# Kernel optimization log

Measured on AMD Instinct MI355X. Metric: run time of the kernel, lower is better.

## Reference

```python
import jax, jax.numpy as jnp
import numpy as np

NEG_SLOPE = 0.2  # PyG GATConv default LeakyReLU slope


def gat_layer(x, src, dst, W, a_src, a_dst, bias, heads, out_dim, concat, n_nodes):
    # x: [N, F_in]; W: [F_in, heads*out_dim]
    h = (x @ W).reshape(n_nodes, heads, out_dim)          # [N, H, C]
    alpha_src = jnp.sum(h * a_src, axis=-1)               # [N, H]
    alpha_dst = jnp.sum(h * a_dst, axis=-1)               # [N, H]
    e = jax.nn.leaky_relu(alpha_src[src] + alpha_dst[dst], NEG_SLOPE)  # [E, H]
    # softmax over edges grouped by destination node (self-loops guarantee nonempty segments)
    m = jax.ops.segment_max(e, dst, num_segments=n_nodes)  # [N, H]
    w = jnp.exp(e - m[dst])
    s = jax.ops.segment_sum(w, dst, num_segments=n_nodes)  # [N, H]
    alpha = w / s[dst]                                     # [E, H]
    msg = h[src] * alpha[:, :, None]                       # [E, H, C]
    out = jax.ops.segment_sum(msg, dst, num_segments=n_nodes)  # [N, H, C]
    if concat:
        out = out.reshape(n_nodes, heads * out_dim)
    else:
        out = out.mean(axis=1)
    return out + bias


def setup_inputs() -> dict:
    key = jax.random.key(0)
    ks = jax.random.split(key, 12)
    N, E = 50000, 600000
    F_IN, OUT = 256, 64
    H1, C1 = 2, 2 * OUT          # conv1: heads=2, per-head dim 128
    F2 = H1 * C1                 # 256
    x = jax.random.normal(ks[0], (N, F_IN), dtype=jnp.float32)
    edge_index = jax.random.randint(ks[1], (2, E), 0, N, dtype=jnp.int64)
    g1 = 1.0 / np.sqrt(F_IN)
    g2 = 1.0 / np.sqrt(F2)
    return {
        "x": x,
        "edge_index": edge_index,
        "W1": jax.random.normal(ks[2], (F_IN, H1 * C1), dtype=jnp.float32) * g1,
        "a1_src": jax.random.normal(ks[3], (H1, C1), dtype=jnp.float32) * g2,
        "a1_dst": jax.random.normal(ks[4], (H1, C1), dtype=jnp.float32) * g2,
        "b1": jnp.zeros((H1 * C1,), dtype=jnp.float32),
        "W2": jax.random.normal(ks[5], (F2, OUT), dtype=jnp.float32) * g2,
        "a2_src": jax.random.normal(ks[6], (1, OUT), dtype=jnp.float32) * 0.1,
        "a2_dst": jax.random.normal(ks[7], (1, OUT), dtype=jnp.float32) * 0.1,
        "b2": jnp.zeros((OUT,), dtype=jnp.float32),
    }


def reference(x, edge_index, W1, a1_src, a1_dst, b1, W2, a2_src, a2_dst, b2):
    N = x.shape[0]
    # add self-loops (PyG GATConv default)
    loops = jnp.arange(N, dtype=edge_index.dtype)
    src = jnp.concatenate([edge_index[0], loops])
    dst = jnp.concatenate([edge_index[1], loops])
    OUT = W2.shape[1]
    h = gat_layer(x, src, dst, W1, a1_src, a1_dst, b1,
                  heads=2, out_dim=2 * OUT, concat=True, n_nodes=N)
    h = jax.nn.elu(h)
    out = gat_layer(h, src, dst, W2, a2_src, a2_dst, b2,
                    heads=1, out_dim=OUT, concat=False, n_nodes=N)
    return out
```

## Files before the change

### kernel.cpp

```cpp
#include <hip/hip_runtime.h>
#include <hip/hip_bf16.h>
#include <math.h>


#define NSLOPE 0.2f

using bf16x8 = __attribute__((ext_vector_type(8))) short;
using f32x4  = __attribute__((ext_vector_type(4))) float;
using u16x8  = __attribute__((ext_vector_type(8))) unsigned short;
using u16x4  = __attribute__((ext_vector_type(4))) unsigned short;

__device__ __forceinline__ unsigned short bf16_rne(float f) {
    unsigned u = __float_as_uint(f);
    return (unsigned short)((u + 0x7FFFu + ((u >> 16) & 1u)) >> 16);
}
__device__ __forceinline__ float bf16_to_f(unsigned short h) {
    return __uint_as_float(((unsigned)h) << 16);
}

__global__ __launch_bounds__(256) void k_prep_all(const float* __restrict__ x,
                                                  const float* __restrict__ W1,
                                                  const float* __restrict__ W2,
                                                  const int* __restrict__ edst,
                                                  unsigned short* __restrict__ Xhi,
                                                  unsigned short* __restrict__ W1hi,
                                                  unsigned short* __restrict__ W1lo,
                                                  unsigned short* __restrict__ W2hi,
                                                  int* __restrict__ deg,
                                                  int BX, int total4, int E) {
    int b = blockIdx.x, t = threadIdx.x;
    if (b < BX) {
        int id = b * 256 + t;
        if (id >= total4) return;
        float4 v = *(const float4*)&x[(size_t)id * 4];
        unsigned short hi[4];
        hi[0] = bf16_rne(v.x); hi[1] = bf16_rne(v.y);
        hi[2] = bf16_rne(v.z); hi[3] = bf16_rne(v.w);
        *(u16x4*)&Xhi[(size_t)id * 4] = *(u16x4*)hi;
    } else if (b < BX + 64) {
        int id = (b - BX) * 256 + t;
        int n = id >> 6, kg = id & 63;
        unsigned short hi[4], lo[4];
#pragma unroll
        for (int c = 0; c < 4; ++c) {
            float w = W1[(kg * 4 + c) * 256 + n];
            unsigned short h = bf16_rne(w);
            hi[c] = h;
            lo[c] = bf16_rne(w - bf16_to_f(h));
        }
        *(u16x4*)&W1hi[n * 256 + kg * 4] = *(u16x4*)hi;
        *(u16x4*)&W1lo[n * 256 + kg * 4] = *(u16x4*)lo;
    } else if (b < BX + 128) {
        int id = (b - BX - 64) * 256 + t;
        int n = id >> 8, k = id & 255;
        W2hi[n * 256 + k] = bf16_rne(W2[k * 64 + n]);
    } else {
        int i = (b - BX - 128) * 256 + t;
        if (i < E) atomicAdd(&deg[edst[i]], 1);
    }
}

__global__ __launch_bounds__(256) void k_scan_ab(const int* __restrict__ deg,
                                                 int* __restrict__ part,
                                                 int* __restrict__ ticket,
                                                 int* __restrict__ off_n,
                                                 int n, int CH) {
    __shared__ int sd[256];
    __shared__ int lastflag;
    int b = blockIdx.x, t = threadIdx.x;
    int s = b * CH, e = min(n, s + CH);
    int loc = 0;
    for (int i = s + t; i < e; i += 256) loc += deg[i] + 1;
    sd[t] = loc;
    __syncthreads();
    for (int o = 128; o > 0; o >>= 1) {
        if (t < o) sd[t] += sd[t + o];
        __syncthreads();
    }
    if (t == 0) {
        part[b] = sd[0];
        __threadfence();
        int old = atomicAdd(ticket, 1);
        lastflag = (old == (int)gridDim.x - 1);
    }
    __syncthreads();
    if (lastflag) {
        __threadfence();
        int v = ((volatile int*)part)[t];
        sd[t] = v;
        __syncthreads();
        for (int o = 1; o < 256; o <<= 1) {
            int u = (t >= o) ? sd[t - o] : 0;
            __syncthreads();
            sd[t] += u;
            __syncthreads();
        }
        part[t] = sd[t] - v;
        if (t == 255) *off_n = sd[255];
    }
}

__global__ __launch_bounds__(256) void k_scan_c(const int* __restrict__ deg,
                                                const int* __restrict__ part,
                                                int* __restrict__ off,
                                                int* __restrict__ cur,
                                                int* __restrict__ srcl, int n, int CH) {
    __shared__ int sd[256];
    int b = blockIdx.x, t = threadIdx.x;
    int s = b * CH, e = min(n, s + CH);
    int base = part[b];
    for (int c = s; c < e; c += 256) {
        int i = c + t;
        int v = (i < e) ? (deg[i] + 1) : 0;
        sd[t] = v;
        __syncthreads();
        for (int o = 1; o < 256; o <<= 1) {
            int u = (t >= o) ? sd[t - o] : 0;
            __syncthreads();
            sd[t] += u;
            __syncthreads();
        }
        if (i < e) {
            int ex = base + sd[t] - v;
            off[i] = ex;
            cur[i] = ex + 1;
            srcl[ex] = i;
        }
        base += sd[255];
        __syncthreads();
    }
}

__global__ void k_fill(const int* __restrict__ src, const int* __restrict__ dst,
                       int* cur, int* __restrict__ srcl, int E) {
    int i = blockIdx.x * blockDim.x + threadIdx.x;
    if (i >= E) return;
    int s = src[i], d = dst[i];
    int p = atomicAdd(&cur[d], 1);
    srcl[p] = s;
}

#define G1S 40
__global__ __launch_bounds__(256) void k_gemm1(const unsigned short* __restrict__ Xhi,
                                               const unsigned short* __restrict__ Whi,
                                               const unsigned short* __restrict__ Wlo,
                                               const float* __restrict__ a1s,
                                               const float* __restrict__ a1d,
                                               unsigned short* __restrict__ h1b,
                                               float* __restrict__ as_,
                                               float* __restrict__ ad_, int M) {
    __shared__ unsigned short sAh[128 * G1S];
    __shared__ unsigned short sBh[128 * G1S], sBl[128 * G1S];
    __shared__ float salS[128][2], salD[128][2];
    int t = threadIdx.x;
    int lane = t & 63, wave = t >> 6;
    int q = lane >> 4, m = lane & 15;
    int row0 = blockIdx.x * 128;
    int head = blockIdx.y;
    int col0 = head * 128;
    int rbase = (wave & 1) * 64, cbase = (wave >> 1) * 64;
    f32x4 acc[4][4];
#pragma unroll
    for (int i = 0; i < 4; ++i)
#pragma unroll
        for (int j = 0; j < 4; ++j) acc[i][j] = (f32x4){0.f, 0.f, 0.f, 0.f};

    for (int kc = 0; kc < 256; kc += 32) {
#pragma unroll
        for (int i2 = 0; i2 < 2; ++i2) {
            int slot = t + i2 * 256;
            int r = slot >> 2, kg = slot & 3;
            int row = row0 + r;
            u16x8 vh = {0, 0, 0, 0, 0, 0, 0, 0};
            if (row < M) vh = *(const u16x8*)&Xhi[(size_t)row * 256 + kc + kg * 8];
            *(u16x8*)&sAh[r * G1S + kg * 8] = vh;
        }
#pragma unroll
        for (int i2 = 0; i2 < 2; ++i2) {
            int slot = t + i2 * 256;
            int n = slot >> 2, kg = slot & 3;
            *(u16x8*)&sBh[n * G1S + kg * 8] =
                *(const u16x8*)&Whi[(size_t)(col0 + n) * 256 + kc + kg * 8];
            *(u16x8*)&sBl[n * G1S + kg * 8] =
                *(const u16x8*)&Wlo[(size_t)(col0 + n) * 256 + kc + kg * 8];
        }
        __syncthreads();
        bf16x8 ah[4], bh[4], bl[4];
#pragma unroll
        for (int i = 0; i < 4; ++i)
            ah[i] = *(bf16x8*)&sAh[(rbase + i * 16 + m) * G1S + q * 8];
#pragma unroll
        for (int j = 0; j < 4; ++j) {
            int r = (cbase + j * 16 + m) * G1S + q * 8;
            bh[j] = *(bf16x8*)&sBh[r];
            bl[j] = *(bf16x8*)&sBl[r];
        }
#pragma unroll
        for (int i = 0; i < 4; ++i)
#pragma unroll
            for (int j = 0; j < 4; ++j) {
                acc[i][j] = __builtin_amdgcn_mfma_f32_16x16x32_bf16(ah[i], bl[j], acc[i][j], 0, 0, 0);
                acc[i][j] = __builtin_amdgcn_mfma_f32_16x16x32_bf16(ah[i], bh[j], acc[i][j], 0, 0, 0);
            }
        __syncthreads();
    }
    float sv[4], dv[4];
#pragma unroll
    for (int j = 0; j < 4; ++j) {
        sv[j] = a1s[head * 128 + cbase + j * 16 + m];
        dv[j] = a1d[head * 128 + cbase + j * 16 + m];
    }
#pragma unroll
    for (int i = 0; i < 4; ++i) {
#pragma unroll
        for (int r = 0; r < 4; ++r) {
            int rl = rbase + i * 16 + q * 4 + r;
            int row = row0 + rl;
            float ps = acc[i][0][r] * sv[0] + acc[i][1][r] * sv[1]
                     + acc[i][2][r] * sv[2] + acc[i][3][r] * sv[3];
            float pd = acc[i][0][r] * dv[0] + acc[i][1][r] * dv[1]
                     + acc[i][2][r] * dv[2] + acc[i][3][r] * dv[3];
#pragma unroll
            for (int mask = 1; mask < 16; mask <<= 1) {
                ps += __shfl_xor(ps, mask, 64);
                pd += __shfl_xor(pd, mask, 64);
            }
            if (m == 0) {
                salS[rl][cbase >> 6] = ps;
                salD[rl][cbase >> 6] = pd;
            }
            if (row < M) {
#pragma unroll
                for (int j = 0; j < 4; ++j)
                    h1b[(size_t)row * 256 + col0 + cbase + j * 16 + m] = bf16_rne(acc[i][j][r]);
            }
        }
    }
    __syncthreads();
    if (t < 128) {
        int row = row0 + t;
        if (row < M) {
            as_[row * 2 + head] = salS[t][0] + salS[t][1];
            ad_[row * 2 + head] = salD[t][0] + salD[t][1];
        }
    }
}

__global__ __launch_bounds__(256) void k_agg1(const unsigned short* __restrict__ h1b,
                                              const float* __restrict__ as,
                                              const float* __restrict__ ad,
                                              const int* __restrict__ off,
                                              const int* __restrict__ srcl,
                                              const float* __restrict__ b1,
                                              unsigned short* __restrict__ helu_b, int N) {
    int wid = (blockIdx.x * blockDim.x + threadIdx.x) >> 6;
    int lane = threadIdx.x & 63;
    if (wid >= N) return;
    int p0 = off[wid], p1 = off[wid + 1];
    float ad0 = ad[wid * 2], ad1 = ad[wid * 2 + 1];
    int half = lane >> 5, hl = lane & 31;
    int headL = hl >> 4;
    float acc[8];
#pragma unroll
    for (int c = 0; c < 8; ++c) acc[c] = 0.f;
    float sumw = 0.f;
    for (int base = p0; base < p1; base += 64) {
        int p = base + lane;
        int cnt = min(64, p1 - base);
        int s = 0; float w0 = 0.f, w1 = 0.f;
        if (p < p1) {
            s = srcl[p];
            float2 av = *(const float2*)&as[s * 2];
            float l0 = av.x + ad0; l0 = l0 >= 0.f ? l0 : NSLOPE * l0;
            float l1 = av.y + ad1; l1 = l1 >= 0.f ? l1 : NSLOPE * l1;
            w0 = __expf(l0); w1 = __expf(l1);
        }
        int pairs = (cnt + 1) >> 1;
        int jj = 0;
        for (; jj + 2 <= pairs; jj += 2) {
            int e0 = 2 * jj + half, e1 = e0 + 2;
            int sa = __shfl(s, e0, 64), sb = __shfl(s, e1, 64);
            float wa0 = __shfl(w0, e0, 64), wa1 = __shfl(w1, e0, 64);
            float wb0 = __shfl(w0, e1, 64), wb1 = __shfl(w1, e1, 64);
            u16x8 hva = *(const u16x8*)&h1b[(size_t)sa * 256 + hl * 8];
            u16x8 hvb = *(const u16x8*)&h1b[(size_t)sb * 256 + hl * 8];
            float wa = headL ? wa1 : wa0;
            float wb = headL ? wb1 : wb0;
            sumw += wa + wb;
#pragma unroll
            for (int c = 0; c < 8; ++c)
                acc[c] += wa * bf16_to_f(hva[c]) + wb * bf16_to_f(hvb[c]);
        }
        for (; jj < pairs; ++jj) {
            int e0 = 2 * jj + half;
            int sa = __shfl(s, e0, 64);
            float wa0 = __shfl(w0, e0, 64), wa1 = __shfl(w1, e0, 64);
            u16x8 hva = *(const u16x8*)&h1b[(size_t)sa * 256 + hl * 8];
            float wa = headL ? wa1 : wa0;
            sumw += wa;
#pragma unroll
            for (int c = 0; c < 8; ++c) acc[c] += wa * bf16_to_f(hva[c]);
        }
    }
#pragma unroll
    for (int c = 0; c < 8; ++c) acc[c] += __shfl_xor(acc[c], 32, 64);
    sumw += __shfl_xor(sumw, 32, 64);
    float inv = 1.0f / sumw;
    int ch = hl * 8 + half * 4;
    float4 bv = *(const float4*)&b1[ch];
    float bb[4] = {bv.x, bv.y, bv.z, bv.w};
    unsigned short o[4];
#pragma unroll
    for (int c = 0; c < 4; ++c) {
        float v = acc[half * 4 + c] * inv + bb[c];
        v = v > 0.f ? v : expm1f(v);
        o[c] = bf16_rne(v);
    }
    *(u16x4*)&helu_b[(size_t)wid * 256 + ch] = *(u16x4*)o;
}

__global__ __launch_bounds__(256) void k_gemm2(const unsigned short* __restrict__ hb,
                                               const unsigned short* __restrict__ Whi,
                                               const float* __restrict__ a2s,
                                               const float* __restrict__ a2d,
                                               unsigned short* __restrict__ h2b,
                                               float* __restrict__ as_,
                                               float* __restrict__ ad_, int M) {
    __shared__ unsigned short sA[128 * G1S];
    __shared__ unsigned short sBh[64 * G1S];
    int t = threadIdx.x;
    int lane = t & 63, wave = t >> 6;
    int q = lane >> 4, m = lane & 15;
    int row0 = blockIdx.x * 128;
    int rbase = wave * 32;
    f32x4 acc[2][4];
#pragma unroll
    for (int i = 0; i < 2; ++i)
#pragma unroll
        for (int j = 0; j < 4; ++j) acc[i][j] = (f32x4){0.f, 0.f, 0.f, 0.f};

    for (int kc = 0; kc < 256; kc += 32) {
#pragma unroll
        for (int i = 0; i < 2; ++i) {
            int slot = t + i * 256;
            int r = slot >> 2, kg = slot & 3;
            int row = row0 + r;
            u16x8 v = {0, 0, 0, 0, 0, 0, 0, 0};
            if (row < M) v = *(const u16x8*)&hb[(size_t)row * 256 + kc + kg * 8];
            *(u16x8*)&sA[r * G1S + kg * 8] = v;
        }
        {
            int n = t >> 2, kg = t & 3;
            *(u16x8*)&sBh[n * G1S + kg * 8] =
                *(const u16x8*)&Whi[(size_t)n * 256 + kc + kg * 8];
        }
        __syncthreads();
        bf16x8 a[2], bh[4];
#pragma unroll
        for (int i = 0; i < 2; ++i)
            a[i] = *(bf16x8*)&sA[(rbase + i * 16 + m) * G1S + q * 8];
#pragma unroll
        for (int j = 0; j < 4; ++j)
            bh[j] = *(bf16x8*)&sBh[(j * 16 + m) * G1S + q * 8];
#pragma unroll
        for (int i = 0; i < 2; ++i)
#pragma unroll
            for (int j = 0; j < 4; ++j)
                acc[i][j] = __builtin_amdgcn_mfma_f32_16x16x32_bf16(a[i], bh[j], acc[i][j], 0, 0, 0);
        __syncthreads();
    }
    float sv[4], dv[4];
#pragma unroll
    for (int j = 0; j < 4; ++j) {
        sv[j] = a2s[j * 16 + m];
        dv[j] = a2d[j * 16 + m];
    }
#pragma unroll
    for (int i = 0; i < 2; ++i) {
#pragma unroll
        for (int r = 0; r < 4; ++r) {
            int row = row0 + rbase + i * 16 + q * 4 + r;
            float ps = acc[i][0][r] * sv[0] + acc[i][1][r] * sv[1]
                     + acc[i][2][r] * sv[2] + acc[i][3][r] * sv[3];
            float pd = acc[i][0][r] * dv[0] + acc[i][1][r] * dv[1]
                     + acc[i][2][r] * dv[2] + acc[i][3][r] * dv[3];
#pragma unroll
            for (int mask = 1; mask < 16; mask <<= 1) {
                ps += __shfl_xor(ps, mask, 64);
                pd += __shfl_xor(pd, mask, 64);
            }
            if (row < M) {
#pragma unroll
                for (int j = 0; j < 4; ++j)
                    h2b[(size_t)row * 64 + j * 16 + m] = bf16_rne(acc[i][j][r]);
                if (m == 0) { as_[row] = ps; ad_[row] = pd; }
            }
        }
    }
}

__global__ __launch_bounds__(256) void k_agg2(const unsigned short* __restrict__ h2b,
                                              const float* __restrict__ as,
                                              const float* __restrict__ ad,
                                              const int* __restrict__ off,
                                              const int* __restrict__ srcl,
                                              const float* __restrict__ b2,
                                              float* __restrict__ out, int N) {
    int wid = (blockIdx.x * blockDim.x + threadIdx.x) >> 6;
    int lane = threadIdx.x & 63;
    if (wid >= N) return;
    int p0 = off[wid], p1 = off[wid + 1];
    float adw = ad[wid];
    int g = lane >> 4, gl = lane & 15;
    float acc[4];
#pragma unroll
    for (int c = 0; c < 4; ++c) acc[c] = 0.f;
    float sumw = 0.f;
    for (int base = p0; base < p1; base += 64) {
        int p = base + lane;
        int cnt = min(64, p1 - base);
        int s = 0; float w = 0.f;
        if (p < p1) {
            s = srcl[p];
            float l = as[s] + adw;
            l = l >= 0.f ? l : NSLOPE * l;
            w = __expf(l);
        }
        int quads = (cnt + 3) >> 2;
        int jj = 0;
        for (; jj + 2 <= quads; jj += 2) {
            int e0 = 4 * jj + g, e1 = e0 + 4;
            int sa = __shfl(s, e0, 64), sb = __shfl(s, e1, 64);
            float wa = __shfl(w, e0, 64), wb = __shfl(w, e1, 64);
            u16x4 hva = *(const u16x4*)&h2b[(size_t)sa * 64 + gl * 4];
            u16x4 hvb = *(const u16x4*)&h2b[(size_t)sb * 64 + gl * 4];
            sumw += wa + wb;
            acc[0] += wa * bf16_to_f(hva.x) + wb * bf16_to_f(hvb.x);
            acc[1] += wa * bf16_to_f(hva.y) + wb * bf16_to_f(hvb.y);
            acc[2] += wa * bf16_to_f(hva.z) + wb * bf16_to_f(hvb.z);
            acc[3] += wa * bf16_to_f(hva.w) + wb * bf16_to_f(hvb.w);
        }
        for (; jj < quads; ++jj) {
            int e0 = 4 * jj + g;
            int sa = __shfl(s, e0, 64);
            float wa = __shfl(w, e0, 64);
            u16x4 hva = *(const u16x4*)&h2b[(size_t)sa * 64 + gl * 4];
            sumw += wa;
            acc[0] += wa * bf16_to_f(hva.x);
            acc[1] += wa * bf16_to_f(hva.y);
            acc[2] += wa * bf16_to_f(hva.z);
            acc[3] += wa * bf16_to_f(hva.w);
        }
    }
#pragma unroll
    for (int c = 0; c < 4; ++c) {
        acc[c] += __shfl_xor(acc[c], 16, 64);
        acc[c] += __shfl_xor(acc[c], 32, 64);
    }
    sumw += __shfl_xor(sumw, 16, 64);
    sumw += __shfl_xor(sumw, 32, 64);
    if (g == 0) {
        float inv = 1.0f / sumw;
        float4 bv = *(const float4*)&b2[gl * 4];
        float4 o;
        o.x = acc[0] * inv + bv.x;
        o.y = acc[1] * inv + bv.y;
        o.z = acc[2] * inv + bv.z;
        o.w = acc[3] * inv + bv.w;
        *(float4*)&out[(size_t)wid * 64 + gl * 4] = o;
    }
}

extern "C" void kernel_launch(void* const* d_in, const int* in_sizes, int n_in,
                              void* d_out, int out_size, void* d_ws, size_t ws_size,
                              hipStream_t stream) {
    if (n_in < 10) return;
    const float* x   = (const float*)d_in[0];
    const int*   ei  = (const int*)d_in[1];
    const float* W1  = (const float*)d_in[2];
    const float* a1s = (const float*)d_in[3];
    const float* a1d = (const float*)d_in[4];
    const float* b1  = (const float*)d_in[5];
    const float* W2  = (const float*)d_in[6];
    const float* a2s = (const float*)d_in[7];
    const float* a2d = (const float*)d_in[8];
    const float* b2  = (const float*)d_in[9];
    float* out = (float*)d_out;

    const int N = in_sizes[0] / 256;
    const int E = in_sizes[1] / 2;
    const int T = E + N;
    const int* esrc = ei;
    const int* edst = ei + E;

    char* ws = (char*)d_ws;
    size_t o = 0;
    auto alloc = [&](size_t bytes) -> void* {
        void* p = ws + o;
        o = (o + bytes + 255) & ~(size_t)255;
        return p;
    };
    size_t szX = (size_t)N * 256 * 2;
    char* regionA = (char*)alloc(szX);
    unsigned short* Xhi    = (unsigned short*)regionA;
    unsigned short* helu_b = (unsigned short*)regionA;

    unsigned short* h1b  = (unsigned short*)alloc((size_t)N * 256 * 2);
    unsigned short* W1hi = (unsigned short*)alloc(256 * 256 * 2);
    unsigned short* W1lo = (unsigned short*)alloc(256 * 256 * 2);
    unsigned short* W2hi = (unsigned short*)alloc(64 * 256 * 2);
    unsigned short* h2b  = (unsigned short*)alloc((size_t)N * 64 * 2);
    float* al1s = (float*)alloc((size_t)N * 2 * 4);
    float* al1d = (float*)alloc((size_t)N * 2 * 4);
    float* al2s = (float*)alloc((size_t)N * 4);
    float* al2d = (float*)alloc((size_t)N * 4);
    int* deg  = (int*)alloc((size_t)(N + 64) * 4);
    int* ticket = deg + N;
    int* off  = (int*)alloc((size_t)(N + 1) * 4);
    int* cur  = (int*)alloc((size_t)N * 4);
    int* part = (int*)alloc(256 * 4);
    int* srcl = (int*)alloc((size_t)T * 4);
    if (o > ws_size) return;

    const int CH = (N + 255) / 256;
    const int total4 = N * 64;
    const int BX = (total4 + 255) / 256;
    const int BH = (E + 255) / 256;

    hipMemsetAsync(deg, 0, (size_t)(N + 64) * 4, stream);
    k_prep_all<<<BX + 128 + BH, 256, 0, stream>>>(x, W1, W2, edst, Xhi,
                                                  W1hi, W1lo, W2hi, deg,
                                                  BX, total4, E);
    k_scan_ab<<<256, 256, 0, stream>>>(deg, part, ticket, &off[N], N, CH);
    k_scan_c<<<256, 256, 0, stream>>>(deg, part, off, cur, srcl, N, CH);
    k_fill<<<(E + 255) / 256, 256, 0, stream>>>(esrc, edst, cur, srcl, E);

    dim3 g1((N + 127) / 128, 2);
    k_gemm1<<<g1, 256, 0, stream>>>(Xhi, W1hi, W1lo, a1s, a1d, h1b, al1s, al1d, N);
    k_agg1<<<(N + 3) / 4, 256, 0, stream>>>(h1b, al1s, al1d, off, srcl, b1, helu_b, N);

    k_gemm2<<<(N + 127) / 128, 256, 0, stream>>>(helu_b, W2hi, a2s, a2d,
                                                 h2b, al2s, al2d, N);
    k_agg2<<<(N + 3) / 4, 256, 0, stream>>>(h2b, al2s, al2d, off, srcl, b2, out, N);
}
```

Baseline: 293.1 us.

## Split edge weight computation into separate edge-parallel kernels before aggregation

```diff
diff --git a/kernel.cpp b/kernel.cpp
--- a/kernel.cpp
+++ b/kernel.cpp
@@ -104,7 +104,8 @@
                                                 const int* __restrict__ part,
                                                 int* __restrict__ off,
                                                 int* __restrict__ cur,
-                                                int* __restrict__ srcl, int n, int CH) {
+                                                int* __restrict__ srcl,
+                                                int* __restrict__ dstl, int n, int CH) {
     __shared__ int sd[256];
     int b = blockIdx.x, t = threadIdx.x;
     int s = b * CH, e = min(n, s + CH);
@@ -125,6 +126,7 @@
             off[i] = ex;
             cur[i] = ex + 1;
             srcl[ex] = i;
+            dstl[ex] = i;
         }
         base += sd[255];
         __syncthreads();
@@ -132,12 +134,13 @@
 }
 
 __global__ void k_fill(const int* __restrict__ src, const int* __restrict__ dst,
-                       int* cur, int* __restrict__ srcl, int E) {
+                       int* cur, int* __restrict__ srcl, int* __restrict__ dstl, int E) {
     int i = blockIdx.x * blockDim.x + threadIdx.x;
     if (i >= E) return;
     int s = src[i], d = dst[i];
     int p = atomicAdd(&cur[d], 1);
     srcl[p] = s;
+    dstl[p] = d;
 }
 
 #define G1S 40
@@ -246,73 +249,80 @@
     }
 }
 
-__global__ __launch_bounds__(256) void k_agg1(const unsigned short* __restrict__ h1b,
-                                              const float* __restrict__ as,
-                                              const float* __restrict__ ad,
-                                              const int* __restrict__ off,
-                                              const int* __restrict__ srcl,
-                                              const float* __restrict__ b1,
-                                              unsigned short* __restrict__ helu_b, int N) {
+__global__ __launch_bounds__(256) void k_edge1(const int* __restrict__ srcl,
+                                               const int* __restrict__ dstl,
+                                               const float* __restrict__ as,
+                                               const float* __restrict__ ad,
+                                               float2* __restrict__ w01, int T) {
+    int p = blockIdx.x * blockDim.x + threadIdx.x;
+    if (p >= T) return;
+    int s = srcl[p], d = dstl[p];
+    float2 av = *(const float2*)&as[s * 2];
+    float2 dv = *(const float2*)&ad[d * 2];
+    float l0 = av.x + dv.x; l0 = l0 >= 0.f ? l0 : NSLOPE * l0;
+    float l1 = av.y + dv.y; l1 = l1 >= 0.f ? l1 : NSLOPE * l1;
+    w01[p] = make_float2(__expf(l0), __expf(l1));
+}
+
+__global__ __launch_bounds__(256) void k_agg1n(const unsigned short* __restrict__ h1b,
+                                               const int* __restrict__ srcl,
+                                               const float2* __restrict__ w01,
+                                               const int* __restrict__ off,
+                                               const float* __restrict__ b1,
+                                               unsigned short* __restrict__ helu_b, int N) {
     int wid = (blockIdx.x * blockDim.x + threadIdx.x) >> 6;
     int lane = threadIdx.x & 63;
     if (wid >= N) return;
     int p0 = off[wid], p1 = off[wid + 1];
-    float ad0 = ad[wid * 2], ad1 = ad[wid * 2 + 1];
-    int half = lane >> 5, hl = lane & 31;
-    int headL = hl >> 4;
-    float acc[8];
-#pragma unroll
-    for (int c = 0; c < 8; ++c) acc[c] = 0.f;
-    float sumw = 0.f;
-    for (int base = p0; base < p1; base += 64) {
-        int p = base + lane;
-        int cnt = min(64, p1 - base);
-        int s = 0; float w0 = 0.f, w1 = 0.f;
-        if (p < p1) {
-            s = srcl[p];
-            float2 av = *(const float2*)&as[s * 2];
-            float l0 = av.x + ad0; l0 = l0 >= 0.f ? l0 : NSLOPE * l0;
-            float l1 = av.y + ad1; l1 = l1 >= 0.f ? l1 : NSLOPE * l1;
-            w0 = __expf(l0); w1 = __expf(l1);
-        }
-        int pairs = (cnt + 1) >> 1;
-        int jj = 0;
-        for (; jj + 2 <= pairs; jj += 2) {
-            int e0 = 2 * jj + half, e1 = e0 + 2;
-            int sa = __shfl(s, e0, 64), sb = __shfl(s, e1, 64);
-            float wa0 = __shfl(w0, e0, 64), wa1 = __shfl(w1, e0, 64);
-            float wb0 = __shfl(w0, e1, 64), wb1 = __shfl(w1, e1, 64);
-            u16x8 hva = *(const u16x8*)&h1b[(size_t)sa * 256 + hl * 8];
-            u16x8 hvb = *(const u16x8*)&h1b[(size_t)sb * 256 + hl * 8];
-            float wa = headL ? wa1 : wa0;
-            float wb = headL ? wb1 : wb0;
-            sumw += wa + wb;
-#pragma unroll
-            for (int c = 0; c < 8; ++c)
-                acc[c] += wa * bf16_to_f(hva[c]) + wb * bf16_to_f(hvb[c]);
-        }
-        for (; jj < pairs; ++jj) {
-            int e0 = 2 * jj + half;
-            int sa = __shfl(s, e0, 64);
-            float wa0 = __shfl(w0, e0, 64), wa1 = __shfl(w1, e0, 64);
-            u16x8 hva = *(const u16x8*)&h1b[(size_t)sa * 256 + hl * 8];
-            float wa = headL ? wa1 : wa0;
-            sumw += wa;
-#pragma unroll
-            for (int c = 0; c < 8; ++c) acc[c] += wa * bf16_to_f(hva[c]);
-        }
-    }
-#pragma unroll
-    for (int c = 0; c < 8; ++c) acc[c] += __shfl_xor(acc[c], 32, 64);
-    sumw += __shfl_xor(sumw, 32, 64);
-    float inv = 1.0f / sumw;
-    int ch = hl * 8 + half * 4;
+    int g = lane >> 4, lc = lane & 15;
+    int hsel = lc >> 3;
+    float acc[16];
+#pragma unroll
+    for (int c = 0; c < 16; ++c) acc[c] = 0.f;
+    float sw = 0.f;
+    for (int eA = p0 + g; eA < p1; eA += 8) {
+        int eB = eA + 4;
+        int sA = srcl[eA];
+        float2 wA = w01[eA];
+        const u16x8* pa = (const u16x8*)&h1b[(size_t)sA * 256 + lc * 16];
+        u16x8 a0 = pa[0], a1 = pa[1];
+        float wa = hsel ? wA.y : wA.x;
+        if (eB < p1) {
+            int sB = srcl[eB];
+            float2 wB = w01[eB];
+            const u16x8* pb = (const u16x8*)&h1b[(size_t)sB * 256 + lc * 16];
+            u16x8 b0 = pb[0], b1v = pb[1];
+            float wb = hsel ? wB.y : wB.x;
+            sw += wa + wb;
+#pragma unroll
+            for (int c = 0; c < 8; ++c) {
+                acc[c]     += wa * bf16_to_f(a0[c]) + wb * bf16_to_f(b0[c]);
+                acc[8 + c] += wa * bf16_to_f(a1[c]) + wb * bf16_to_f(b1v[c]);
+            }
+        } else {
+            sw += wa;
+#pragma unroll
+            for (int c = 0; c < 8; ++c) {
+                acc[c]     += wa * bf16_to_f(a0[c]);
+                acc[8 + c] += wa * bf16_to_f(a1[c]);
+            }
+        }
+    }
+#pragma unroll
+    for (int c = 0; c < 16; ++c) {
+        acc[c] += __shfl_xor(acc[c], 16, 64);
+        acc[c] += __shfl_xor(acc[c], 32, 64);
+    }
+    sw += __shfl_xor(sw, 16, 64);
+    sw += __shfl_xor(sw, 32, 64);
+    float inv = 1.0f / sw;
+    int ch = lc * 16 + g * 4;
     float4 bv = *(const float4*)&b1[ch];
     float bb[4] = {bv.x, bv.y, bv.z, bv.w};
     unsigned short o[4];
 #pragma unroll
     for (int c = 0; c < 4; ++c) {
-        float v = acc[half * 4 + c] * inv + bb[c];
+        float v = acc[g * 4 + c] * inv + bb[c];
         v = v > 0.f ? v : expm1f(v);
         o[c] = bf16_rne(v);
     }
@@ -399,57 +409,52 @@
     }
 }
 
-__global__ __launch_bounds__(256) void k_agg2(const unsigned short* __restrict__ h2b,
-                                              const float* __restrict__ as,
-                                              const float* __restrict__ ad,
-                                              const int* __restrict__ off,
-                                              const int* __restrict__ srcl,
-                                              const float* __restrict__ b2,
-                                              float* __restrict__ out, int N) {
+__global__ __launch_bounds__(256) void k_edge2(const int* __restrict__ srcl,
+                                               const int* __restrict__ dstl,
+                                               const float* __restrict__ as,
+                                               const float* __restrict__ ad,
+                                               float* __restrict__ w2l, int T) {
+    int p = blockIdx.x * blockDim.x + threadIdx.x;
+    if (p >= T) return;
+    int s = srcl[p], d = dstl[p];
+    float l = as[s] + ad[d];
+    l = l >= 0.f ? l : NSLOPE * l;
+    w2l[p] = __expf(l);
+}
+
+__global__ __launch_bounds__(256) void k_agg2n(const unsigned short* __restrict__ h2b,
+                                               const int* __restrict__ srcl,
+                                               const float* __restrict__ w2l,
+                                               const int* __restrict__ off,
+                                               const float* __restrict__ b2,
+                                               float* __restrict__ out, int N) {
     int wid = (blockIdx.x * blockDim.x + threadIdx.x) >> 6;
     int lane = threadIdx.x & 63;
     if (wid >= N) return;
     int p0 = off[wid], p1 = off[wid + 1];
-    float adw = ad[wid];
-    int g = lane >> 4, gl = lane & 15;
-    float acc[4];
-#pragma unroll
-    for (int c = 0; c < 4; ++c) acc[c] = 0.f;
-    float sumw = 0.f;
-    for (int base = p0; base < p1; base += 64) {
-        int p = base + lane;
-        int cnt = min(64, p1 - base);
-        int s = 0; float w = 0.f;
-        if (p < p1) {
-            s = srcl[p];
-            float l = as[s] + adw;
-            l = l >= 0.f ? l : NSLOPE * l;
-            w = __expf(l);
-        }
-        int quads = (cnt + 3) >> 2;
-        int jj = 0;
-        for (; jj + 2 <= quads; jj += 2) {
-            int e0 = 4 * jj + g, e1 = e0 + 4;
-            int sa = __shfl(s, e0, 64), sb = __shfl(s, e1, 64);
-            float wa = __shfl(w, e0, 64), wb = __shfl(w, e1, 64);
-            u16x4 hva = *(const u16x4*)&h2b[(size_t)sa * 64 + gl * 4];
-            u16x4 hvb = *(const u16x4*)&h2b[(size_t)sb * 64 + gl * 4];
-            sumw += wa + wb;
-            acc[0] += wa * bf16_to_f(hva.x) + wb * bf16_to_f(hvb.x);
-            acc[1] += wa * bf16_to_f(hva.y) + wb * bf16_to_f(hvb.y);
-            acc[2] += wa * bf16_to_f(hva.z) + wb * bf16_to_f(hvb.z);
-            acc[3] += wa * bf16_to_f(hva.w) + wb * bf16_to_f(hvb.w);
-        }
-        for (; jj < quads; ++jj) {
-            int e0 = 4 * jj + g;
-            int sa = __shfl(s, e0, 64);
-            float wa = __shfl(w, e0, 64);
-            u16x4 hva = *(const u16x4*)&h2b[(size_t)sa * 64 + gl * 4];
-            sumw += wa;
-            acc[0] += wa * bf16_to_f(hva.x);
-            acc[1] += wa * bf16_to_f(hva.y);
-            acc[2] += wa * bf16_to_f(hva.z);
-            acc[3] += wa * bf16_to_f(hva.w);
+    int g = lane >> 4, lc = lane & 15;
+    float acc[4] = {0.f, 0.f, 0.f, 0.f};
+    float sw = 0.f;
+    for (int eA = p0 + g; eA < p1; eA += 8) {
+        int eB = eA + 4;
+        int sA = srcl[eA];
+        float wa = w2l[eA];
+        u16x4 ha = *(const u16x4*)&h2b[(size_t)sA * 64 + lc * 4];
+        if (eB < p1) {
+            int sB = srcl[eB];
+            float wb = w2l[eB];
+            u16x4 hb = *(const u16x4*)&h2b[(size_t)sB * 64 + lc * 4];
+            sw += wa + wb;
+            acc[0] += wa * bf16_to_f(ha.x) + wb * bf16_to_f(hb.x);
+            acc[1] += wa * bf16_to_f(ha.y) + wb * bf16_to_f(hb.y);
+            acc[2] += wa * bf16_to_f(ha.z) + wb * bf16_to_f(hb.z);
+            acc[3] += wa * bf16_to_f(ha.w) + wb * bf16_to_f(hb.w);
+        } else {
+            sw += wa;
+            acc[0] += wa * bf16_to_f(ha.x);
+            acc[1] += wa * bf16_to_f(ha.y);
+            acc[2] += wa * bf16_to_f(ha.z);
+            acc[3] += wa * bf16_to_f(ha.w);
         }
     }
 #pragma unroll
@@ -457,17 +462,17 @@
         acc[c] += __shfl_xor(acc[c], 16, 64);
         acc[c] += __shfl_xor(acc[c], 32, 64);
     }
-    sumw += __shfl_xor(sumw, 16, 64);
-    sumw += __shfl_xor(sumw, 32, 64);
+    sw += __shfl_xor(sw, 16, 64);
+    sw += __shfl_xor(sw, 32, 64);
     if (g == 0) {
-        float inv = 1.0f / sumw;
-        float4 bv = *(const float4*)&b2[gl * 4];
+        float inv = 1.0f / sw;
+        float4 bv = *(const float4*)&b2[lc * 4];
         float4 o;
         o.x = acc[0] * inv + bv.x;
         o.y = acc[1] * inv + bv.y;
         o.z = acc[2] * inv + bv.z;
         o.w = acc[3] * inv + bv.w;
-        *(float4*)&out[(size_t)wid * 64 + gl * 4] = o;
+        *(float4*)&out[(size_t)wid * 64 + lc * 4] = o;
     }
 }
 
@@ -520,26 +525,32 @@
     int* cur  = (int*)alloc((size_t)N * 4);
     int* part = (int*)alloc(256 * 4);
     int* srcl = (int*)alloc((size_t)T * 4);
+    int* dstl = (int*)alloc((size_t)T * 4);
+    float2* w01 = (float2*)alloc((size_t)T * 8);
+    float* w2l  = (float*)alloc((size_t)T * 4);
     if (o > ws_size) return;
 
     const int CH = (N + 255) / 256;
     const int total4 = N * 64;
     const int BX = (total4 + 255) / 256;
     const int BH = (E + 255) / 256;
+    const int BT = (T + 255) / 256;
 
     hipMemsetAsync(deg, 0, (size_t)(N + 64) * 4, stream);
     k_prep_all<<<BX + 128 + BH, 256, 0, stream>>>(x, W1, W2, edst, Xhi,
                                                   W1hi, W1lo, W2hi, deg,
                                                   BX, total4, E);
     k_scan_ab<<<256, 256, 0, stream>>>(deg, part, ticket, &off[N], N, CH);
-    k_scan_c<<<256, 256, 0, stream>>>(deg, part, off, cur, srcl, N, CH);
-    k_fill<<<(E + 255) / 256, 256, 0, stream>>>(esrc, edst, cur, srcl, E);
+    k_scan_c<<<256, 256, 0, stream>>>(deg, part, off, cur, srcl, dstl, N, CH);
+    k_fill<<<(E + 255) / 256, 256, 0, stream>>>(esrc, edst, cur, srcl, dstl, E);
 
     dim3 g1((N + 127) / 128, 2);
     k_gemm1<<<g1, 256, 0, stream>>>(Xhi, W1hi, W1lo, a1s, a1d, h1b, al1s, al1d, N);
-    k_agg1<<<(N + 3) / 4, 256, 0, stream>>>(h1b, al1s, al1d, off, srcl, b1, helu_b, N);
+    k_edge1<<<BT, 256, 0, stream>>>(srcl, dstl, al1s, al1d, w01, T);
+    k_agg1n<<<(N + 3) / 4, 256, 0, stream>>>(h1b, srcl, w01, off, b1, helu_b, N);
 
     k_gemm2<<<(N + 127) / 128, 256, 0, stream>>>(helu_b, W2hi, a2s, a2d,
                                                  h2b, al2s, al2d, N);
-    k_agg2<<<(N + 3) / 4, 256, 0, stream>>>(h2b, al2s, al2d, off, srcl, b2, out, N);
-}
+    k_edge2<<<BT, 256, 0, stream>>>(srcl, dstl, al2s, al2d, w2l, T);
+    k_agg2n<<<(N + 3) / 4, 256, 0, stream>>>(h2b, srcl, w2l, off, b2, out, N);
+}
```

New measurement: 317.0 us. +8.2%, slower.

## Split edge attention weight computation into separate per-edge kernels before aggregation

Applied to the files above, without the earlier changes.

```diff
diff --git a/kernel.cpp b/kernel.cpp
--- a/kernel.cpp
+++ b/kernel.cpp
@@ -104,7 +104,8 @@
                                                 const int* __restrict__ part,
                                                 int* __restrict__ off,
                                                 int* __restrict__ cur,
-                                                int* __restrict__ srcl, int n, int CH) {
+                                                int* __restrict__ srcl,
+                                                int* __restrict__ dstl, int n, int CH) {
     __shared__ int sd[256];
     int b = blockIdx.x, t = threadIdx.x;
     int s = b * CH, e = min(n, s + CH);
@@ -125,6 +126,7 @@
             off[i] = ex;
             cur[i] = ex + 1;
             srcl[ex] = i;
+            dstl[ex] = i;
         }
         base += sd[255];
         __syncthreads();
@@ -132,12 +134,13 @@
 }
 
 __global__ void k_fill(const int* __restrict__ src, const int* __restrict__ dst,
-                       int* cur, int* __restrict__ srcl, int E) {
+                       int* cur, int* __restrict__ srcl, int* __restrict__ dstl, int E) {
     int i = blockIdx.x * blockDim.x + threadIdx.x;
     if (i >= E) return;
     int s = src[i], d = dst[i];
     int p = atomicAdd(&cur[d], 1);
     srcl[p] = s;
+    dstl[p] = d;
 }
 
 #define G1S 40
@@ -246,9 +249,23 @@
     }
 }
 
+__global__ __launch_bounds__(256) void k_edge1(const int* __restrict__ srcl,
+                                               const int* __restrict__ dstl,
+                                               const float* __restrict__ as,
+                                               const float* __restrict__ ad,
+                                               float2* __restrict__ w01, int T) {
+    int p = blockIdx.x * blockDim.x + threadIdx.x;
+    if (p >= T) return;
+    int s = srcl[p], d = dstl[p];
+    float2 av = *(const float2*)&as[s * 2];
+    float2 dv = *(const float2*)&ad[d * 2];
+    float l0 = av.x + dv.x; l0 = l0 >= 0.f ? l0 : NSLOPE * l0;
+    float l1 = av.y + dv.y; l1 = l1 >= 0.f ? l1 : NSLOPE * l1;
+    w01[p] = make_float2(__expf(l0), __expf(l1));
+}
+
 __global__ __launch_bounds__(256) void k_agg1(const unsigned short* __restrict__ h1b,
-                                              const float* __restrict__ as,
-                                              const float* __restrict__ ad,
+                                              const float2* __restrict__ w01,
                                               const int* __restrict__ off,
                                               const int* __restrict__ srcl,
                                               const float* __restrict__ b1,
@@ -257,7 +274,6 @@
     int lane = threadIdx.x & 63;
     if (wid >= N) return;
     int p0 = off[wid], p1 = off[wid + 1];
-    float ad0 = ad[wid * 2], ad1 = ad[wid * 2 + 1];
     int half = lane >> 5, hl = lane & 31;
     int headL = hl >> 4;
     float acc[8];
@@ -270,10 +286,8 @@
         int s = 0; float w0 = 0.f, w1 = 0.f;
         if (p < p1) {
             s = srcl[p];
-            float2 av = *(const float2*)&as[s * 2];
-            float l0 = av.x + ad0; l0 = l0 >= 0.f ? l0 : NSLOPE * l0;
-            float l1 = av.y + ad1; l1 = l1 >= 0.f ? l1 : NSLOPE * l1;
-            w0 = __expf(l0); w1 = __expf(l1);
+            float2 wv = w01[p];
+            w0 = wv.x; w1 = wv.y;
         }
         int pairs = (cnt + 1) >> 1;
         int jj = 0;
@@ -399,9 +413,21 @@
     }
 }
 
+__global__ __launch_bounds__(256) void k_edge2(const int* __restrict__ srcl,
+                                               const int* __restrict__ dstl,
+                                               const float* __restrict__ as,
+                                               const float* __restrict__ ad,
+                                               float* __restrict__ w2l, int T) {
+    int p = blockIdx.x * blockDim.x + threadIdx.x;
+    if (p >= T) return;
+    int s = srcl[p], d = dstl[p];
+    float l = as[s] + ad[d];
+    l = l >= 0.f ? l : NSLOPE * l;
+    w2l[p] = __expf(l);
+}
+
 __global__ __launch_bounds__(256) void k_agg2(const unsigned short* __restrict__ h2b,
-                                              const float* __restrict__ as,
-                                              const float* __restrict__ ad,
+                                              const float* __restrict__ w2l,
                                               const int* __restrict__ off,
                                               const int* __restrict__ srcl,
                                               const float* __restrict__ b2,
@@ -410,7 +436,6 @@
     int lane = threadIdx.x & 63;
     if (wid >= N) return;
     int p0 = off[wid], p1 = off[wid + 1];
-    float adw = ad[wid];
     int g = lane >> 4, gl = lane & 15;
     float acc[4];
 #pragma unroll
@@ -422,9 +447,7 @@
         int s = 0; float w = 0.f;
         if (p < p1) {
             s = srcl[p];
-            float l = as[s] + adw;
-            l = l >= 0.f ? l : NSLOPE * l;
-            w = __expf(l);
+            w = w2l[p];
         }
         int quads = (cnt + 3) >> 2;
         int jj = 0;
@@ -520,26 +543,32 @@
     int* cur  = (int*)alloc((size_t)N * 4);
     int* part = (int*)alloc(256 * 4);
     int* srcl = (int*)alloc((size_t)T * 4);
+    int* dstl = (int*)alloc((size_t)T * 4);
+    float2* w01 = (float2*)alloc((size_t)T * 8);
+    float* w2l  = (float*)alloc((size_t)T * 4);
     if (o > ws_size) return;
 
     const int CH = (N + 255) / 256;
     const int total4 = N * 64;
     const int BX = (total4 + 255) / 256;
     const int BH = (E + 255) / 256;
+    const int BT = (T + 255) / 256;
 
     hipMemsetAsync(deg, 0, (size_t)(N + 64) * 4, stream);
     k_prep_all<<<BX + 128 + BH, 256, 0, stream>>>(x, W1, W2, edst, Xhi,
                                                   W1hi, W1lo, W2hi, deg,
                                                   BX, total4, E);
     k_scan_ab<<<256, 256, 0, stream>>>(deg, part, ticket, &off[N], N, CH);
-    k_scan_c<<<256, 256, 0, stream>>>(deg, part, off, cur, srcl, N, CH);
-    k_fill<<<(E + 255) / 256, 256, 0, stream>>>(esrc, edst, cur, srcl, E);
+    k_scan_c<<<256, 256, 0, stream>>>(deg, part, off, cur, srcl, dstl, N, CH);
+    k_fill<<<(E + 255) / 256, 256, 0, stream>>>(esrc, edst, cur, srcl, dstl, E);
 
     dim3 g1((N + 127) / 128, 2);
     k_gemm1<<<g1, 256, 0, stream>>>(Xhi, W1hi, W1lo, a1s, a1d, h1b, al1s, al1d, N);
-    k_agg1<<<(N + 3) / 4, 256, 0, stream>>>(h1b, al1s, al1d, off, srcl, b1, helu_b, N);
+    k_edge1<<<BT, 256, 0, stream>>>(srcl, dstl, al1s, al1d, w01, T);
+    k_agg1<<<(N + 3) / 4, 256, 0, stream>>>(h1b, w01, off, srcl, b1, helu_b, N);
 
     k_gemm2<<<(N + 127) / 128, 256, 0, stream>>>(helu_b, W2hi, a2s, a2d,
                                                  h2b, al2s, al2d, N);
-    k_agg2<<<(N + 3) / 4, 256, 0, stream>>>(h2b, al2s, al2d, off, srcl, b2, out, N);
-}
+    k_edge2<<<BT, 256, 0, stream>>>(srcl, dstl, al2s, al2d, w2l, T);
+    k_agg2<<<(N + 3) / 4, 256, 0, stream>>>(h2b, w2l, off, srcl, b2, out, N);
+}
```

Result: slower. 302.7 us (+3.3%).
